# Performance work log

Measured on AMD Instinct MI355X. Metric: run time of the kernel, lower is better.

Reference implementation:

```python
import math
import jax, jax.numpy as jnp
import numpy as np
from jax import lax

C = 64          # channels
N = 16          # d_state
EXPAND = 2
DI = C * EXPAND # d_inner = 128
K = 4           # d_conv
DT_RANK = math.ceil(C / 16)  # 4


def setup_inputs() -> dict:
    key = jax.random.key(0)
    ks = jax.random.split(key, 8)
    B, D, H, W = 1, 48, 48, 48
    s = 0.02
    x = jax.random.normal(ks[0], (B, C, D, H, W), jnp.float32)
    # stacked params for the 3 directional MambaBlocks (z, y, x)
    in_proj = jax.random.normal(ks[1], (3, 2 * DI, C), jnp.float32) * s
    conv_w = jax.random.normal(ks[2], (3, DI, 1, K), jnp.float32) * s
    conv_b = jnp.zeros((3, DI), jnp.float32)
    x_proj = jax.random.normal(ks[3], (3, DT_RANK + 2 * N, DI), jnp.float32) * s
    dt_w = jax.random.normal(ks[4], (3, DI, DT_RANK), jnp.float32) * s
    dt_b = jax.random.normal(ks[5], (3, DI), jnp.float32) * s
    A_log = jnp.log(jnp.broadcast_to(jnp.arange(1, N + 1, dtype=jnp.float32), (3, DI, N)))
    D_ssm = jnp.ones((3, DI), jnp.float32)
    out_proj = jax.random.normal(ks[6], (3, C, DI), jnp.float32) * s
    ln_g = jnp.ones((3, C), jnp.float32)
    ln_b = jnp.zeros((3, C), jnp.float32)
    alpha = jnp.ones((3,), jnp.float32)
    return dict(x=x, in_proj=in_proj, conv_w=conv_w, conv_b=conv_b, x_proj=x_proj,
                dt_w=dt_w, dt_b=dt_b, A_log=A_log, D_ssm=D_ssm, out_proj=out_proj,
                ln_g=ln_g, ln_b=ln_b, alpha=alpha)


def _layer_norm(x, g, b, eps=1e-5):
    m = x.mean(-1, keepdims=True)
    v = ((x - m) ** 2).mean(-1, keepdims=True)
    return (x - m) * lax.rsqrt(v + eps) * g + b


def _mamba(xs, in_w, cw, cb, xp, dtw, dtb, a_log, d_p, ow):
    # xs: (b, l, C)
    b, l, _ = xs.shape
    xr = xs @ in_w.T                              # (b, l, 2*DI)
    xin, res = jnp.split(xr, 2, axis=-1)
    # depthwise causal conv1d (torch pads K-1 both sides then slices [:l])
    xc = lax.conv_general_dilated(xin, cw.transpose(2, 1, 0), (1,), [(K - 1, 0)],
                                  dimension_numbers=('NWC', 'WIO', 'NWC'),
                                  feature_group_count=DI) + cb
    u = jax.nn.silu(xc)                           # (b, l, DI)
    x_dbl = u @ xp.T                              # (b, l, DT_RANK + 2N)
    dlt = x_dbl[..., :DT_RANK]
    Bm = x_dbl[..., DT_RANK:DT_RANK + N]
    Cm = x_dbl[..., DT_RANK + N:]
    delta = jax.nn.softplus(dlt @ dtw.T + dtb)    # (b, l, DI)
    A = -jnp.exp(a_log)                           # (DI, N)

    def step(h, inp):
        d_t, B_t, C_t, u_t = inp                  # (b,DI),(b,N),(b,N),(b,DI)
        h = jnp.exp(d_t[:, :, None] * A) * h + (d_t * u_t)[:, :, None] * B_t[:, None, :]
        return h, jnp.einsum('bdn,bn->bd', h, C_t)

    h0 = jnp.zeros((b, DI, N), xs.dtype)
    _, ys = lax.scan(step, h0, (jnp.swapaxes(delta, 0, 1), jnp.swapaxes(Bm, 0, 1),
                                jnp.swapaxes(Cm, 0, 1), jnp.swapaxes(u, 0, 1)))
    y = jnp.swapaxes(ys, 0, 1) + u * d_p          # (b, l, DI)
    y = y * jax.nn.silu(res)
    return y @ ow.T                               # (b, l, C)


def reference(x, in_proj, conv_w, conv_b, x_proj, dt_w, dt_b, A_log, D_ssm,
              out_proj, ln_g, ln_b, alpha):
    B, Cc, D, H, W = x.shape

    def run(i, xseq):
        xn = _layer_norm(xseq, ln_g[i], ln_b[i])
        return _mamba(xn, in_proj[i], conv_w[i], conv_b[i], x_proj[i],
                      dt_w[i], dt_b[i], A_log[i], D_ssm[i], out_proj[i])

    xz = run(0, x.transpose(0, 3, 4, 2, 1).reshape(B * H * W, D, Cc))
    xz = xz.reshape(B, H, W, D, Cc).transpose(0, 4, 3, 1, 2)
    xy = run(1, x.transpose(0, 2, 4, 3, 1).reshape(B * D * W, H, Cc))
    xy = xy.reshape(B, D, W, H, Cc).transpose(0, 4, 1, 3, 2)
    xx = run(2, x.transpose(0, 2, 3, 4, 1).reshape(B * D * H, W, Cc))
    xx = xx.reshape(B, D, H, W, Cc).transpose(0, 4, 1, 2, 3)
    w = jax.nn.softmax(alpha)
    return w[0] * xz + w[1] * xy + w[2] * xx
```

## Files before the change

kernel.cpp:

```cpp
#include <hip/hip_runtime.h>
#include <math.h>


#define CS   110592
#define L2E  1.44269504088896340736f

#define IPT_OFF  (110592 * 256)
#define OPT_OFF  (IPT_OFF + 3 * 64 * 256)
#define WS_FLOATS (OPT_OFF + 3 * 128 * 64)

__device__ __forceinline__ float fast_silu(float x) {
    return x / (1.0f + __expf(-x));
}

__global__ void prep_kernel(const float* __restrict__ ip,
                            const float* __restrict__ op,
                            float* __restrict__ ws)
{
    float* ipT = ws + IPT_OFF;
    float* opT = ws + OPT_OFF;
    int i = blockIdx.x * 256 + threadIdx.x;
    if (i < 3 * 256 * 64) {
        int dir = i / 16384, r = i % 16384, j = r / 64, c = r % 64;
        ipT[dir * 16384 + c * 256 + j] = ip[i];
    } else {
        int k = i - 3 * 256 * 64;
        if (k < 3 * 64 * 128) {
            int dir = k / 8192, r = k % 8192, c = r / 128, dch = r % 128;
            opT[dir * 8192 + dch * 64 + c] = op[k];
        }
    }
}

template<int DIR>
__global__ __launch_bounds__(256, 4)
void k1_lnproj(const float* __restrict__ x,
               const float* __restrict__ ln_g,
               const float* __restrict__ ln_b,
               float* __restrict__ ws)
{
    __shared__ float Xs[64 * 64];
    const float* ipT = ws + IPT_OFF + DIR * 16384;
    float* tb = ws;
    const int tid = threadIdx.x;
    const int p0 = blockIdx.x * 64;

    {
        const int c0 = tid >> 6, j = tid & 63;
#pragma unroll
        for (int cc = 0; cc < 16; cc++) {
            int c = cc * 4 + c0;
            Xs[c * 64 + j] = x[c * CS + p0 + j];
        }
    }
    __syncthreads();

    if (tid < 64) {
        float s1 = 0.f, s2 = 0.f;
#pragma unroll
        for (int c = 0; c < 64; c++) {
            float v = Xs[c * 64 + tid];
            s1 += v; s2 += v * v;
        }
        float m  = s1 * (1.f / 64.f);
        float rs = rsqrtf(s2 * (1.f / 64.f) - m * m + 1e-5f);
#pragma unroll
        for (int c = 0; c < 64; c++) {
            Xs[c * 64 + tid] = (Xs[c * 64 + tid] - m) * rs * ln_g[DIR * 64 + c]
                               + ln_b[DIR * 64 + c];
        }
    }
    __syncthreads();

    float wgt[64];
#pragma unroll
    for (int c = 0; c < 64; c++) wgt[c] = ipT[c * 256 + tid];

    for (int g = 0; g < 4; g++) {
        float acc[16];
#pragma unroll
        for (int i = 0; i < 16; i++) acc[i] = 0.f;
#pragma unroll 8
        for (int c = 0; c < 64; c++) {
            const float4* xr = (const float4*)&Xs[c * 64 + g * 16];
            float4 x0 = xr[0], x1 = xr[1], x2 = xr[2], x3 = xr[3];
            float wv = wgt[c];
            acc[0]  += x0.x * wv; acc[1]  += x0.y * wv;
            acc[2]  += x0.z * wv; acc[3]  += x0.w * wv;
            acc[4]  += x1.x * wv; acc[5]  += x1.y * wv;
            acc[6]  += x1.z * wv; acc[7]  += x1.w * wv;
            acc[8]  += x2.x * wv; acc[9]  += x2.y * wv;
            acc[10] += x2.z * wv; acc[11] += x2.w * wv;
            acc[12] += x3.x * wv; acc[13] += x3.y * wv;
            acc[14] += x3.z * wv; acc[15] += x3.w * wv;
        }
        if (tid >= 128) {
#pragma unroll
            for (int i = 0; i < 16; i++) acc[i] = fast_silu(acc[i]);
        }
#pragma unroll
        for (int i = 0; i < 16; i++) {
            int p = p0 + g * 16 + i;
            int d_sp = p / 2304, rem = p % 2304;
            int h = rem / 48, w = rem % 48;
            int tau;
            if (DIR == 0)      tau = rem * 48 + d_sp;
            else if (DIR == 1) tau = (d_sp * 48 + w) * 48 + h;
            else               tau = (d_sp * 48 + h) * 48 + w;
            tb[tau * 256 + tid] = acc[i];
        }
    }
}

template<int DIR>
__global__ __launch_bounds__(128, 2)
void k2_scan(const float* __restrict__ conv_w,
             const float* __restrict__ conv_b,
             const float* __restrict__ x_proj,
             const float* __restrict__ dt_w,
             const float* __restrict__ dt_b,
             const float* __restrict__ A_log,
             const float* __restrict__ D_ssm,
             float* __restrict__ ws)
{
    __shared__ float u_s[48 * 132];
    __shared__ float xd_s[48 * 44];
    float* tb = ws;
    const int tid = threadIdx.x;
    const int t0 = blockIdx.x * (48 * 256);

    {
        const int d = tid;
        float xin[48];
#pragma unroll
        for (int t = 0; t < 48; t++) xin[t] = tb[t0 + t * 256 + d];
        float4 cw = *(const float4*)(conv_w + DIR * 512 + d * 4);
        float cb  = conv_b[DIR * 128 + d];
#pragma unroll
        for (int t = 0; t < 48; t++) {
            float a0 = (t >= 3) ? xin[t-3] : 0.f;
            float a1 = (t >= 2) ? xin[t-2] : 0.f;
            float a2 = (t >= 1) ? xin[t-1] : 0.f;
            float v = cw.x * a0 + cw.y * a1 + cw.z * a2 + cw.w * xin[t] + cb;
            u_s[t * 132 + d] = fast_silu(v);
        }
    }
    __syncthreads();

    {
        const int t = tid & 63;
        const int wv = __builtin_amdgcn_readfirstlane(tid >> 6);
        if (t < 48) {
            float acc[18];
#pragma unroll
            for (int j = 0; j < 18; j++) acc[j] = 0.f;
            const float* xpw = x_proj + DIR * 36 * 128 + (wv * 18) * 128;
#pragma unroll
            for (int qc = 0; qc < 4; qc++) {
                float4 u4[8];
                const float4* urow = (const float4*)&u_s[t * 132 + qc * 32];
#pragma unroll
                for (int q = 0; q < 8; q++) u4[q] = urow[q];
#pragma unroll
                for (int j = 0; j < 18; j++) {
                    const float4* wr = (const float4*)(xpw + j * 128 + qc * 32);
                    float a0 = 0.f, a1 = 0.f, a2 = 0.f, a3 = 0.f;
#pragma unroll
                    for (int q = 0; q < 8; q++) {
                        float4 w4 = wr[q];
                        a0 += u4[q].x * w4.x; a1 += u4[q].y * w4.y;
                        a2 += u4[q].z * w4.z; a3 += u4[q].w * w4.w;
                    }
                    acc[j] += (a0 + a1) + (a2 + a3);
                }
            }
#pragma unroll
            for (int j = 0; j < 18; j++) xd_s[t * 44 + wv * 18 + j] = acc[j];
        }
    }
    __syncthreads();

    {
        const int d = tid;
        float A2[16]; bool powok = true;
#pragma unroll
        for (int n = 0; n < 16; n++) {
            float a = -__expf(A_log[DIR * 2048 + d * 16 + n]);
            powok = powok && (fabsf(a + (float)(n + 1)) < 1e-3f);
            A2[n] = a * L2E;
        }
        float4 dtw = *(const float4*)(dt_w + DIR * 512 + d * 4);
        float dtbv = dt_b[DIR * 128 + d];
        float dsv  = D_ssm[DIR * 128 + d];
        float h[16];
#pragma unroll
        for (int n = 0; n < 16; n++) h[n] = 0.f;

#define HN(n, Bc, Cc) h[n] = e[n] * h[n] + du * (Bc); y += h[n] * (Cc);
#define SCAN_BODY(EXP_BLOCK)                                                   \
        for (int tt = 0; tt < 48; tt++) {                                      \
            const float4* xr4 = (const float4*)&xd_s[tt * 44];                 \
            float4 dv = xr4[0];                                                \
            float uu = u_s[tt * 132 + d];                                      \
            float dl = dtbv + dtw.x*dv.x + dtw.y*dv.y + dtw.z*dv.z + dtw.w*dv.w; \
            float delta = (dl > 20.f) ? dl : log1pf(__expf(dl));               \
            float du = delta * uu;                                             \
            float e[16];                                                       \
            EXP_BLOCK                                                          \
            float4 B0 = xr4[1], B1 = xr4[2], B2 = xr4[3], B3 = xr4[4];         \
            float4 C0 = xr4[5], C1 = xr4[6], C2 = xr4[7], C3 = xr4[8];         \
            float y = 0.f;                                                     \
            HN(0,  B0.x, C0.x) HN(1,  B0.y, C0.y)                              \
            HN(2,  B0.z, C0.z) HN(3,  B0.w, C0.w)                              \
            HN(4,  B1.x, C1.x) HN(5,  B1.y, C1.y)                              \
            HN(6,  B1.z, C1.z) HN(7,  B1.w, C1.w)                              \
            HN(8,  B2.x, C2.x) HN(9,  B2.y, C2.y)                              \
            HN(10, B2.z, C2.z) HN(11, B2.w, C2.w)                              \
            HN(12, B3.x, C3.x) HN(13, B3.y, C3.y)                              \
            HN(14, B3.z, C3.z) HN(15, B3.w, C3.w)                              \
            tb[t0 + tt * 256 + d] = y + uu * dsv;                              \
        }

        if (powok) {
            SCAN_BODY({
                float p = exp2f(-delta * L2E);
                e[0] = p;
                _Pragma("unroll")
                for (int n = 1; n < 16; n++) e[n] = e[n-1] * p;
            })
        } else {
            SCAN_BODY({
                _Pragma("unroll")
                for (int n = 0; n < 16; n++) e[n] = exp2f(delta * A2[n]);
            })
        }
#undef SCAN_BODY
#undef HN
    }
}

template<int DIR, bool FIRST>
__global__ __launch_bounds__(128, 4)
void k3_outproj(const float* __restrict__ alpha,
                float* __restrict__ ws,
                float* __restrict__ out)
{
    __shared__ float sb[48 * 132];
    float* tb = ws;
    const float* opT = ws + OPT_OFF + DIR * 8192;
    const int tid = threadIdx.x;
    const int b = blockIdx.x;
    const int d_sp = b / 48;
    const int h = b - d_sp * 48;

    float a0 = alpha[0], a1 = alpha[1], a2 = alpha[2];
    float mx = fmaxf(a0, fmaxf(a1, a2));
    float e0 = __expf(a0 - mx), e1 = __expf(a1 - mx), e2 = __expf(a2 - mx);
    float wdir = ((DIR == 0) ? e0 : (DIR == 1) ? e1 : e2) / (e0 + e1 + e2);

#pragma unroll 4
    for (int w = 0; w < 48; w++) {
        int tau;
        if (DIR == 0)      tau = (h * 48 + w) * 48 + d_sp;
        else if (DIR == 1) tau = (d_sp * 48 + w) * 48 + h;
        else               tau = (d_sp * 48 + h) * 48 + w;
        float zv = tb[tau * 256 + tid];
        float rv = tb[tau * 256 + 128 + tid];
        sb[w * 132 + tid] = zv * rv;
    }
    __syncthreads();

    const int cp = tid & 31;
    const int wg = tid >> 5;
    float acc0[12], acc1[12];
#pragma unroll
    for (int i = 0; i < 12; i++) { acc0[i] = 0.f; acc1[i] = 0.f; }
#pragma unroll 2
    for (int dc = 0; dc < 32; dc++) {
        float w0[4], w1[4];
#pragma unroll
        for (int i = 0; i < 4; i++) {
            w0[i] = opT[(dc * 4 + i) * 64 + cp];
            w1[i] = opT[(dc * 4 + i) * 64 + cp + 32];
        }
#pragma unroll
        for (int i = 0; i < 12; i++) {
            int w = wg * 12 + i;
            float4 z4 = *(const float4*)&sb[w * 132 + dc * 4];
            acc0[i] += z4.x * w0[0] + z4.y * w0[1] + z4.z * w0[2] + z4.w * w0[3];
            acc1[i] += z4.x * w1[0] + z4.y * w1[1] + z4.z * w1[2] + z4.w * w1[3];
        }
    }
    __syncthreads();
#pragma unroll
    for (int i = 0; i < 12; i++) {
        int w = wg * 12 + i;
        sb[cp * 49 + w]        = acc0[i];
        sb[(cp + 32) * 49 + w] = acc1[i];
    }
    __syncthreads();
    const int obase = d_sp * 2304 + h * 48;
    for (int o = tid; o < 3072; o += 128) {
        int c = o / 48, w = o - c * 48;
        int addr = c * CS + obase + w;
        float val = wdir * sb[c * 49 + w];
        if (!FIRST) val += out[addr];
        out[addr] = val;
    }
}

template<int DIR, bool FIRST>
__global__ __launch_bounds__(128, 2)
void mamba_dir_v1(const float* __restrict__ x, const float* __restrict__ in_proj,
                  const float* __restrict__ conv_w, const float* __restrict__ conv_b,
                  const float* __restrict__ x_proj, const float* __restrict__ dt_w,
                  const float* __restrict__ dt_b, const float* __restrict__ A_log,
                  const float* __restrict__ D_ssm, const float* __restrict__ out_proj,
                  const float* __restrict__ ln_g, const float* __restrict__ ln_b,
                  const float* __restrict__ alpha, float* __restrict__ out)
{
    __shared__ float xs_s[48 * 68];
    __shared__ float u_s[48 * 128];
    __shared__ float xd_s[48 * 40];
    const int tid = threadIdx.x;
    const int lane = tid & 63;
    const int wv = __builtin_amdgcn_readfirstlane(tid >> 6);
    const int s = blockIdx.x;
    int base, TS;
    if (DIR == 0)      { base = s;                               TS = 2304; }
    else if (DIR == 1) { base = (s / 48) * 2304 + (s % 48);      TS = 48;   }
    else               { base = (s / 48) * 2304 + (s % 48) * 48; TS = 1;    }
    const float* ip = in_proj + DIR * 256 * 64;
    const float* xp = x_proj + DIR * 36 * 128;
    const float* op = out_proj + DIR * 64 * 128;
    float a0 = alpha[0], a1 = alpha[1], a2 = alpha[2];
    float mx = fmaxf(a0, fmaxf(a1, a2));
    float e0 = __expf(a0 - mx), e1 = __expf(a1 - mx), e2 = __expf(a2 - mx);
    float wdir = ((DIR == 0) ? e0 : (DIR == 1) ? e1 : e2) / (e0 + e1 + e2);
    for (int o = tid; o < 48 * 64; o += 128) {
        int t = o % 48, c = o / 48;
        xs_s[t * 68 + c] = x[c * CS + base + t * TS];
    }
    __syncthreads();
    const int t = lane;
    float xr[64];
    if (t < 48) {
        const float4* row = (const float4*)&xs_s[t * 68];
#pragma unroll
        for (int q = 0; q < 16; q++) {
            float4 v = row[q];
            xr[4*q+0]=v.x; xr[4*q+1]=v.y; xr[4*q+2]=v.z; xr[4*q+3]=v.w;
        }
        float m = 0.f;
#pragma unroll
        for (int c = 0; c < 64; c++) m += xr[c];
        m *= (1.0f / 64.0f);
        float var = 0.f;
#pragma unroll
        for (int c = 0; c < 64; c++) { float d0 = xr[c] - m; var += d0 * d0; }
        var *= (1.0f / 64.0f);
        float rs = rsqrtf(var + 1e-5f);
#pragma unroll
        for (int c = 0; c < 64; c++)
            xr[c] = (xr[c] - m) * rs * ln_g[DIR * 64 + c] + ln_b[DIR * 64 + c];
    }
    __syncthreads();
    if (t < 48 && wv == 0) {
        float4* row = (float4*)&xs_s[t * 68];
#pragma unroll
        for (int q = 0; q < 16; q++) {
            float4 v; v.x=xr[4*q+0]; v.y=xr[4*q+1]; v.z=xr[4*q+2]; v.w=xr[4*q+3];
            row[q] = v;
        }
    }
    if (t < 48) {
        for (int jj = 0; jj < 64; jj++) {
            int j = wv * 64 + jj;
            const float4* wrow = (const float4*)(ip + j * 64);
            float acc = 0.f;
#pragma unroll
            for (int q = 0; q < 16; q++) {
                float4 w4 = wrow[q];
                acc += xr[4*q+0]*w4.x + xr[4*q+1]*w4.y + xr[4*q+2]*w4.z + xr[4*q+3]*w4.w;
            }
            int col = (((j >> 2) ^ (t & 7)) << 2) | (j & 3);
            u_s[t * 128 + col] = acc;
        }
    }
    __syncthreads();
    {
        const int d = tid;
        float4 cw = *(const float4*)(conv_w + DIR * 512 + d * 4);
        float cb = conv_b[DIR * 128 + d];
        float w0 = 0.f, w1 = 0.f, w2 = 0.f;
        for (int tt = 0; tt < 48; tt++) {
            int col = tt * 128 + ((((d >> 2) ^ (tt & 7)) << 2) | (d & 3));
            float w3 = u_s[col];
            float xc = cw.x*w0 + cw.y*w1 + cw.z*w2 + cw.w*w3 + cb;
            u_s[col] = fast_silu(xc);
            w0 = w1; w1 = w2; w2 = w3;
        }
    }
    __syncthreads();
    if (t < 48) {
        float ur[128];
        const float4* urow = (const float4*)&u_s[t * 128];
#pragma unroll
        for (int g = 0; g < 32; g++) {
            float4 v = urow[g ^ (t & 7)];
            ur[4*g]=v.x; ur[4*g+1]=v.y; ur[4*g+2]=v.z; ur[4*g+3]=v.w;
        }
        for (int jj = 0; jj < 18; jj++) {
            int j = wv * 18 + jj;
            const float4* wrow = (const float4*)(xp + j * 128);
            float acc = 0.f;
#pragma unroll
            for (int q = 0; q < 32; q++) {
                float4 w4 = wrow[q];
                acc += ur[4*q]*w4.x + ur[4*q+1]*w4.y + ur[4*q+2]*w4.z + ur[4*q+3]*w4.w;
            }
            xd_s[t * 40 + j] = acc;
        }
    }
    __syncthreads();
    {
        const int d = tid;
        float A2[16]; bool powok = true;
#pragma unroll
        for (int n = 0; n < 16; n++) {
            float a = -__expf(A_log[DIR * 2048 + d * 16 + n]);
            powok = powok && (fabsf(a + (float)(n + 1)) < 1e-3f);
            A2[n] = a * L2E;
        }
        float4 dtw = *(const float4*)(dt_w + DIR * 512 + d * 4);
        float dtbv = dt_b[DIR * 128 + d];
        float dsv = D_ssm[DIR * 128 + d];
        float h[16];
#pragma unroll
        for (int n = 0; n < 16; n++) h[n] = 0.f;
#define SCAN_BODY(EXP_BLOCK)                                                   \
        for (int tt = 0; tt < 48; tt++) {                                      \
            const float* xrow = &xd_s[tt * 40];                                \
            float4 dl4 = *(const float4*)xrow;                                 \
            float dl = dtbv + dtw.x*dl4.x + dtw.y*dl4.y + dtw.z*dl4.z + dtw.w*dl4.w; \
            float delta = (dl > 20.f) ? dl : log1pf(__expf(dl));               \
            int col = tt * 128 + ((((d >> 2) ^ (tt & 7)) << 2) | (d & 3));     \
            float uu = u_s[col];                                               \
            float du = delta * uu;                                             \
            float e[16];                                                       \
            EXP_BLOCK                                                          \
            float4 Bv0 = *(const float4*)(xrow + 4);                           \
            float4 Bv1 = *(const float4*)(xrow + 8);                           \
            float4 Bv2 = *(const float4*)(xrow + 12);                          \
            float4 Bv3 = *(const float4*)(xrow + 16);                          \
            float4 Cv0 = *(const float4*)(xrow + 20);                          \
            float4 Cv1 = *(const float4*)(xrow + 24);                          \
            float4 Cv2 = *(const float4*)(xrow + 28);                          \
            float4 Cv3 = *(const float4*)(xrow + 32);                          \
            float Bf[16] = {Bv0.x,Bv0.y,Bv0.z,Bv0.w, Bv1.x,Bv1.y,Bv1.z,Bv1.w,  \
                            Bv2.x,Bv2.y,Bv2.z,Bv2.w, Bv3.x,Bv3.y,Bv3.z,Bv3.w}; \
            float Cf[16] = {Cv0.x,Cv0.y,Cv0.z,Cv0.w, Cv1.x,Cv1.y,Cv1.z,Cv1.w,  \
                            Cv2.x,Cv2.y,Cv2.z,Cv2.w, Cv3.x,Cv3.y,Cv3.z,Cv3.w}; \
            float y = 0.f;                                                     \
            _Pragma("unroll")                                                  \
            for (int n = 0; n < 16; n++) {                                     \
                h[n] = e[n] * h[n] + du * Bf[n];                               \
                y += h[n] * Cf[n];                                             \
            }                                                                  \
            u_s[col] = y + uu * dsv;                                           \
        }
        if (powok) {
            SCAN_BODY({
                float p = exp2f(-delta * L2E);
                e[0] = p;
                _Pragma("unroll")
                for (int n = 1; n < 16; n++) e[n] = e[n-1] * p;
            })
        } else {
            SCAN_BODY({
                _Pragma("unroll")
                for (int n = 0; n < 16; n++) e[n] = exp2f(delta * A2[n]);
            })
        }
#undef SCAN_BODY
    }
    {
        const int d = tid;
        float wr[64];
        const float4* wrow = (const float4*)(ip + (128 + d) * 64);
#pragma unroll
        for (int q = 0; q < 16; q++) {
            float4 v = wrow[q];
            wr[4*q]=v.x; wr[4*q+1]=v.y; wr[4*q+2]=v.z; wr[4*q+3]=v.w;
        }
        for (int tt = 0; tt < 48; tt++) {
            const float4* xrow = (const float4*)&xs_s[tt * 68];
            float acc = 0.f;
#pragma unroll
            for (int q = 0; q < 16; q++) {
                float4 v = xrow[q];
                acc += v.x*wr[4*q] + v.y*wr[4*q+1] + v.z*wr[4*q+2] + v.w*wr[4*q+3];
            }
            int col = tt * 128 + ((((d >> 2) ^ (tt & 7)) << 2) | (d & 3));
            u_s[col] = u_s[col] * fast_silu(acc);
        }
    }
    __syncthreads();
    if (t < 48) {
        float zr[128];
        const float4* zrow = (const float4*)&u_s[t * 128];
#pragma unroll
        for (int g = 0; g < 32; g++) {
            float4 v = zrow[g ^ (t & 7)];
            zr[4*g]=v.x; zr[4*g+1]=v.y; zr[4*g+2]=v.z; zr[4*g+3]=v.w;
        }
        for (int cc = 0; cc < 32; cc++) {
            int c = wv * 32 + cc;
            const float4* wrow = (const float4*)(op + c * 128);
            float acc = 0.f;
#pragma unroll
            for (int q = 0; q < 32; q++) {
                float4 w4 = wrow[q];
                acc += zr[4*q]*w4.x + zr[4*q+1]*w4.y + zr[4*q+2]*w4.z + zr[4*q+3]*w4.w;
            }
            int oaddr = c * CS + base + t * TS;
            float vout = wdir * acc;
            if (!FIRST) vout += out[oaddr];
            out[oaddr] = vout;
        }
    }
}

extern "C" void kernel_launch(void* const* d_in, const int* in_sizes, int n_in,
                              void* d_out, int out_size, void* d_ws, size_t ws_size,
                              hipStream_t stream) {
    const float* x        = (const float*)d_in[0];
    const float* in_proj  = (const float*)d_in[1];
    const float* conv_w   = (const float*)d_in[2];
    const float* conv_b   = (const float*)d_in[3];
    const float* x_proj   = (const float*)d_in[4];
    const float* dt_w     = (const float*)d_in[5];
    const float* dt_b     = (const float*)d_in[6];
    const float* A_log    = (const float*)d_in[7];
    const float* D_ssm    = (const float*)d_in[8];
    const float* out_proj = (const float*)d_in[9];
    const float* ln_g     = (const float*)d_in[10];
    const float* ln_b     = (const float*)d_in[11];
    const float* alpha    = (const float*)d_in[12];
    float* out = (float*)d_out;
    float* ws  = (float*)d_ws;

    if (ws_size >= (size_t)WS_FLOATS * 4) {
        prep_kernel<<<288, 256, 0, stream>>>(in_proj, out_proj, ws);

        k1_lnproj<0><<<1728, 256, 0, stream>>>(x, ln_g, ln_b, ws);
        k2_scan<0><<<2304, 128, 0, stream>>>(conv_w, conv_b, x_proj, dt_w, dt_b, A_log, D_ssm, ws);
        k3_outproj<0, true ><<<2304, 128, 0, stream>>>(alpha, ws, out);

        k1_lnproj<1><<<1728, 256, 0, stream>>>(x, ln_g, ln_b, ws);
        k2_scan<1><<<2304, 128, 0, stream>>>(conv_w, conv_b, x_proj, dt_w, dt_b, A_log, D_ssm, ws);
        k3_outproj<1, false><<<2304, 128, 0, stream>>>(alpha, ws, out);

        k1_lnproj<2><<<1728, 256, 0, stream>>>(x, ln_g, ln_b, ws);
        k2_scan<2><<<2304, 128, 0, stream>>>(conv_w, conv_b, x_proj, dt_w, dt_b, A_log, D_ssm, ws);
        k3_outproj<2, false><<<2304, 128, 0, stream>>>(alpha, ws, out);
    } else {
        dim3 grid(2304), block(128);
        mamba_dir_v1<0, true ><<<grid, block, 0, stream>>>(x, in_proj, conv_w, conv_b, x_proj,
            dt_w, dt_b, A_log, D_ssm, out_proj, ln_g, ln_b, alpha, out);
        mamba_dir_v1<1, false><<<grid, block, 0, stream>>>(x, in_proj, conv_w, conv_b, x_proj,
            dt_w, dt_b, A_log, D_ssm, out_proj, ln_g, ln_b, alpha, out);
        mamba_dir_v1<2, false><<<grid, block, 0, stream>>>(x, in_proj, conv_w, conv_b, x_proj,
            dt_w, dt_b, A_log, D_ssm, out_proj, ln_g, ln_b, alpha, out);
    }
}
```

Baseline: 1.128 ms.

## Recompute gate projection in outproj and halve the intermediate buffer

k1 now computes only the 128 x-branch channels and stores them in natural spatial order at 128 floats per position, instead of 256 in a scan-transposed order. k3 recomputes layernorm and the gate (res) half of the in_proj so that half no longer round-trips through global memory. k2 reads its 48-step sequences with a direction-dependent stride, uses an XOR-swizzled shared layout instead of padding, and computes exp per state with a branch-free softplus, dropping the power-chain fast path. The intent is to cut global memory traffic, at the cost of extra recomputation, strided loads in k2, and more transcendentals in the scan.

```diff
diff --git a/kernel.cpp b/kernel.cpp
--- a/kernel.cpp
+++ b/kernel.cpp
@@ -3,14 +3,17 @@
 
 
 #define CS   110592
-#define L2E  1.44269504088896340736f
-
-#define IPT_OFF  (110592 * 256)
+#define TBF  (110592 * 128)
+#define IPT_OFF  TBF
 #define OPT_OFF  (IPT_OFF + 3 * 64 * 256)
 #define WS_FLOATS (OPT_OFF + 3 * 128 * 64)
 
 __device__ __forceinline__ float fast_silu(float x) {
     return x / (1.0f + __expf(-x));
+}
+__device__ __forceinline__ float softplus_f(float x) {
+    float em = __expf(-fabsf(x));
+    return fmaxf(x, 0.f) + __logf(1.f + em);
 }
 
 __global__ void prep_kernel(const float* __restrict__ ip,
@@ -72,11 +75,14 @@
     }
     __syncthreads();
 
+    const int ch = tid & 127, half = tid >> 7;
     float wgt[64];
 #pragma unroll
-    for (int c = 0; c < 64; c++) wgt[c] = ipT[c * 256 + tid];
-
-    for (int g = 0; g < 4; g++) {
+    for (int c = 0; c < 64; c++) wgt[c] = ipT[c * 256 + ch];
+
+#pragma unroll
+    for (int gg = 0; gg < 2; gg++) {
+        int g = half * 2 + gg;
         float acc[16];
 #pragma unroll
         for (int i = 0; i < 16; i++) acc[i] = 0.f;
@@ -94,21 +100,9 @@
             acc[12] += x3.x * wv; acc[13] += x3.y * wv;
             acc[14] += x3.z * wv; acc[15] += x3.w * wv;
         }
-        if (tid >= 128) {
-#pragma unroll
-            for (int i = 0; i < 16; i++) acc[i] = fast_silu(acc[i]);
-        }
-#pragma unroll
-        for (int i = 0; i < 16; i++) {
-            int p = p0 + g * 16 + i;
-            int d_sp = p / 2304, rem = p % 2304;
-            int h = rem / 48, w = rem % 48;
-            int tau;
-            if (DIR == 0)      tau = rem * 48 + d_sp;
-            else if (DIR == 1) tau = (d_sp * 48 + w) * 48 + h;
-            else               tau = (d_sp * 48 + h) * 48 + w;
-            tb[tau * 256 + tid] = acc[i];
-        }
+#pragma unroll
+        for (int i = 0; i < 16; i++)
+            tb[(size_t)(p0 + g * 16 + i) * 128 + ch] = acc[i];
     }
 }
 
@@ -123,17 +117,23 @@
              const float* __restrict__ D_ssm,
              float* __restrict__ ws)
 {
-    __shared__ float u_s[48 * 132];
-    __shared__ float xd_s[48 * 44];
+    __shared__ float u_s[48 * 128];
+    __shared__ float xd_s[48 * 36];
     float* tb = ws;
     const int tid = threadIdx.x;
-    const int t0 = blockIdx.x * (48 * 256);
+    const int s = blockIdx.x;
+
+    int base, TS;
+    if (DIR == 0)      { base = s;                               TS = 2304; }
+    else if (DIR == 1) { base = (s / 48) * 2304 + (s % 48);      TS = 48;   }
+    else               { base = (s / 48) * 2304 + (s % 48) * 48; TS = 1;    }
 
     {
         const int d = tid;
         float xin[48];
 #pragma unroll
-        for (int t = 0; t < 48; t++) xin[t] = tb[t0 + t * 256 + d];
+        for (int t = 0; t < 48; t++)
+            xin[t] = tb[(size_t)(base + t * TS) * 128 + d];
         float4 cw = *(const float4*)(conv_w + DIR * 512 + d * 4);
         float cb  = conv_b[DIR * 128 + d];
 #pragma unroll
@@ -142,52 +142,57 @@
             float a1 = (t >= 2) ? xin[t-2] : 0.f;
             float a2 = (t >= 1) ? xin[t-1] : 0.f;
             float v = cw.x * a0 + cw.y * a1 + cw.z * a2 + cw.w * xin[t] + cb;
-            u_s[t * 132 + d] = fast_silu(v);
-        }
-    }
-    __syncthreads();
-
-    {
-        const int t = tid & 63;
+            u_s[t * 128 + (((((d >> 2) ^ (t & 7))) << 2) | (d & 3))] = fast_silu(v);
+        }
+    }
+    __syncthreads();
+
+    {
+        const int t  = tid & 63;
         const int wv = __builtin_amdgcn_readfirstlane(tid >> 6);
+        const int tr = (t < 48) ? t : 47;
+        const int sw = tr & 7;
+        float acc[18];
+#pragma unroll
+        for (int j = 0; j < 18; j++) acc[j] = 0.f;
+        const float* xpw = x_proj + DIR * 36 * 128 + (wv * 18) * 128;
+        const float4* urow = (const float4*)&u_s[tr * 128];
+#pragma unroll
+        for (int qc = 0; qc < 4; qc++) {
+            float4 u4[8];
+#pragma unroll
+            for (int q = 0; q < 8; q++) u4[q] = urow[qc * 8 + (q ^ sw)];
+#pragma unroll
+            for (int j = 0; j < 18; j++) {
+                const float4* wr = (const float4*)(xpw + j * 128 + qc * 32);
+                float a0 = 0.f, a1 = 0.f, a2 = 0.f, a3 = 0.f;
+#pragma unroll
+                for (int q = 0; q < 8; q++) {
+                    float4 w4 = wr[q];
+                    a0 += u4[q].x * w4.x; a1 += u4[q].y * w4.y;
+                    a2 += u4[q].z * w4.z; a3 += u4[q].w * w4.w;
+                }
+                acc[j] += (a0 + a1) + (a2 + a3);
+            }
+        }
         if (t < 48) {
-            float acc[18];
-#pragma unroll
-            for (int j = 0; j < 18; j++) acc[j] = 0.f;
-            const float* xpw = x_proj + DIR * 36 * 128 + (wv * 18) * 128;
-#pragma unroll
-            for (int qc = 0; qc < 4; qc++) {
-                float4 u4[8];
-                const float4* urow = (const float4*)&u_s[t * 132 + qc * 32];
-#pragma unroll
-                for (int q = 0; q < 8; q++) u4[q] = urow[q];
-#pragma unroll
-                for (int j = 0; j < 18; j++) {
-                    const float4* wr = (const float4*)(xpw + j * 128 + qc * 32);
-                    float a0 = 0.f, a1 = 0.f, a2 = 0.f, a3 = 0.f;
-#pragma unroll
-                    for (int q = 0; q < 8; q++) {
-                        float4 w4 = wr[q];
-                        a0 += u4[q].x * w4.x; a1 += u4[q].y * w4.y;
-                        a2 += u4[q].z * w4.z; a3 += u4[q].w * w4.w;
-                    }
-                    acc[j] += (a0 + a1) + (a2 + a3);
-                }
-            }
-#pragma unroll
-            for (int j = 0; j < 18; j++) xd_s[t * 44 + wv * 18 + j] = acc[j];
+#pragma unroll
+            for (int j = 0; j < 18; j++) xd_s[t * 36 + wv * 18 + j] = acc[j];
         }
     }
     __syncthreads();
 
     {
         const int d = tid;
-        float A2[16]; bool powok = true;
-#pragma unroll
-        for (int n = 0; n < 16; n++) {
-            float a = -__expf(A_log[DIR * 2048 + d * 16 + n]);
-            powok = powok && (fabsf(a + (float)(n + 1)) < 1e-3f);
-            A2[n] = a * L2E;
+        float A[16];
+        {
+            const float4* al = (const float4*)(A_log + DIR * 2048 + d * 16);
+#pragma unroll
+            for (int q = 0; q < 4; q++) {
+                float4 v = al[q];
+                A[4*q+0] = -__expf(v.x); A[4*q+1] = -__expf(v.y);
+                A[4*q+2] = -__expf(v.z); A[4*q+3] = -__expf(v.w);
+            }
         }
         float4 dtw = *(const float4*)(dt_w + DIR * 512 + d * 4);
         float dtbv = dt_b[DIR * 128 + d];
@@ -196,77 +201,112 @@
 #pragma unroll
         for (int n = 0; n < 16; n++) h[n] = 0.f;
 
-#define HN(n, Bc, Cc) h[n] = e[n] * h[n] + du * (Bc); y += h[n] * (Cc);
-#define SCAN_BODY(EXP_BLOCK)                                                   \
-        for (int tt = 0; tt < 48; tt++) {                                      \
-            const float4* xr4 = (const float4*)&xd_s[tt * 44];                 \
-            float4 dv = xr4[0];                                                \
-            float uu = u_s[tt * 132 + d];                                      \
-            float dl = dtbv + dtw.x*dv.x + dtw.y*dv.y + dtw.z*dv.z + dtw.w*dv.w; \
-            float delta = (dl > 20.f) ? dl : log1pf(__expf(dl));               \
-            float du = delta * uu;                                             \
-            float e[16];                                                       \
-            EXP_BLOCK                                                          \
-            float4 B0 = xr4[1], B1 = xr4[2], B2 = xr4[3], B3 = xr4[4];         \
-            float4 C0 = xr4[5], C1 = xr4[6], C2 = xr4[7], C3 = xr4[8];         \
-            float y = 0.f;                                                     \
-            HN(0,  B0.x, C0.x) HN(1,  B0.y, C0.y)                              \
-            HN(2,  B0.z, C0.z) HN(3,  B0.w, C0.w)                              \
-            HN(4,  B1.x, C1.x) HN(5,  B1.y, C1.y)                              \
-            HN(6,  B1.z, C1.z) HN(7,  B1.w, C1.w)                              \
-            HN(8,  B2.x, C2.x) HN(9,  B2.y, C2.y)                              \
-            HN(10, B2.z, C2.z) HN(11, B2.w, C2.w)                              \
-            HN(12, B3.x, C3.x) HN(13, B3.y, C3.y)                              \
-            HN(14, B3.z, C3.z) HN(15, B3.w, C3.w)                              \
-            tb[t0 + tt * 256 + d] = y + uu * dsv;                              \
-        }
-
-        if (powok) {
-            SCAN_BODY({
-                float p = exp2f(-delta * L2E);
-                e[0] = p;
-                _Pragma("unroll")
-                for (int n = 1; n < 16; n++) e[n] = e[n-1] * p;
-            })
-        } else {
-            SCAN_BODY({
-                _Pragma("unroll")
-                for (int n = 0; n < 16; n++) e[n] = exp2f(delta * A2[n]);
-            })
-        }
-#undef SCAN_BODY
+        const int dsw_hi = d >> 2, dlo = d & 3;
+        for (int tt = 0; tt < 48; tt++) {
+            const float4* xr4 = (const float4*)&xd_s[tt * 36];
+            float4 R0 = xr4[0];
+            float uu = u_s[tt * 128 + (((dsw_hi ^ (tt & 7)) << 2) | dlo)];
+            float dl = dtbv + dtw.x*R0.x + dtw.y*R0.y + dtw.z*R0.z + dtw.w*R0.w;
+            float delta = softplus_f(dl);
+            float du = delta * uu;
+            float4 B0 = xr4[1], B1 = xr4[2], B2 = xr4[3], B3 = xr4[4];
+            float4 C0 = xr4[5], C1 = xr4[6], C2 = xr4[7], C3 = xr4[8];
+            float y0 = 0.f, y1 = 0.f, y2 = 0.f, y3 = 0.f;
+#define HN(n, Bc, Cc, ya) { float e = __expf(delta * A[n]); \
+            h[n] = e * h[n] + du * (Bc); ya += h[n] * (Cc); }
+            HN(0,  B0.x, C0.x, y0) HN(1,  B0.y, C0.y, y1)
+            HN(2,  B0.z, C0.z, y2) HN(3,  B0.w, C0.w, y3)
+            HN(4,  B1.x, C1.x, y0) HN(5,  B1.y, C1.y, y1)
+            HN(6,  B1.z, C1.z, y2) HN(7,  B1.w, C1.w, y3)
+            HN(8,  B2.x, C2.x, y0) HN(9,  B2.y, C2.y, y1)
+            HN(10, B2.z, C2.z, y2) HN(11, B2.w, C2.w, y3)
+            HN(12, B3.x, C3.x, y0) HN(13, B3.y, C3.y, y1)
+            HN(14, B3.z, C3.z, y2) HN(15, B3.w, C3.w, y3)
 #undef HN
+            tb[(size_t)(base + tt * TS) * 128 + d] =
+                ((y0 + y1) + (y2 + y3)) + uu * dsv;
+        }
     }
 }
 
 template<int DIR, bool FIRST>
 __global__ __launch_bounds__(128, 4)
-void k3_outproj(const float* __restrict__ alpha,
+void k3_outproj(const float* __restrict__ x,
+                const float* __restrict__ ln_g,
+                const float* __restrict__ ln_b,
+                const float* __restrict__ alpha,
                 float* __restrict__ ws,
                 float* __restrict__ out)
 {
     __shared__ float sb[48 * 132];
+    __shared__ float xs[64 * 52];
     float* tb = ws;
+    const float* ipT = ws + IPT_OFF + DIR * 16384;
     const float* opT = ws + OPT_OFF + DIR * 8192;
     const int tid = threadIdx.x;
     const int b = blockIdx.x;
     const int d_sp = b / 48;
     const int h = b - d_sp * 48;
+    const int obase = d_sp * 2304 + h * 48;
 
     float a0 = alpha[0], a1 = alpha[1], a2 = alpha[2];
     float mx = fmaxf(a0, fmaxf(a1, a2));
     float e0 = __expf(a0 - mx), e1 = __expf(a1 - mx), e2 = __expf(a2 - mx);
     float wdir = ((DIR == 0) ? e0 : (DIR == 1) ? e1 : e2) / (e0 + e1 + e2);
 
-#pragma unroll 4
-    for (int w = 0; w < 48; w++) {
-        int tau;
-        if (DIR == 0)      tau = (h * 48 + w) * 48 + d_sp;
-        else if (DIR == 1) tau = (d_sp * 48 + w) * 48 + h;
-        else               tau = (d_sp * 48 + h) * 48 + w;
-        float zv = tb[tau * 256 + tid];
-        float rv = tb[tau * 256 + 128 + tid];
-        sb[w * 132 + tid] = zv * rv;
+    for (int o = tid; o < 64 * 48; o += 128) {
+        int c = o / 48, w = o - c * 48;
+        xs[c * 52 + w] = x[c * CS + obase + w];
+    }
+    __syncthreads();
+
+    if (tid < 48) {
+        const int w = tid;
+        float s1 = 0.f, s2 = 0.f;
+#pragma unroll
+        for (int c = 0; c < 64; c++) {
+            float v = xs[c * 52 + w];
+            s1 += v; s2 += v * v;
+        }
+        float m  = s1 * (1.f / 64.f);
+        float rs = rsqrtf(s2 * (1.f / 64.f) - m * m + 1e-5f);
+#pragma unroll
+        for (int c = 0; c < 64; c++) {
+            xs[c * 52 + w] = (xs[c * 52 + w] - m) * rs * ln_g[DIR * 64 + c]
+                             + ln_b[DIR * 64 + c];
+        }
+    }
+    __syncthreads();
+
+    {
+        const int d = tid;
+        float wgt2[64];
+#pragma unroll
+        for (int c = 0; c < 64; c++) wgt2[c] = ipT[c * 256 + 128 + d];
+#pragma unroll
+        for (int wb = 0; wb < 4; wb++) {
+            float acc[12];
+#pragma unroll
+            for (int i = 0; i < 12; i++) acc[i] = 0.f;
+#pragma unroll 8
+            for (int c = 0; c < 64; c++) {
+                const float4* xr = (const float4*)&xs[c * 52 + wb * 12];
+                float4 v0 = xr[0], v1 = xr[1], v2 = xr[2];
+                float wv = wgt2[c];
+                acc[0] += v0.x * wv; acc[1] += v0.y * wv;
+                acc[2] += v0.z * wv; acc[3] += v0.w * wv;
+                acc[4] += v1.x * wv; acc[5] += v1.y * wv;
+                acc[6] += v1.z * wv; acc[7] += v1.w * wv;
+                acc[8] += v2.x * wv; acc[9] += v2.y * wv;
+                acc[10] += v2.z * wv; acc[11] += v2.w * wv;
+            }
+#pragma unroll
+            for (int i = 0; i < 12; i++) {
+                int w = wb * 12 + i;
+                float zv = tb[(size_t)(obase + w) * 128 + d];
+                sb[w * 132 + d] = zv * fast_silu(acc[i]);
+            }
+        }
     }
     __syncthreads();
 
@@ -299,7 +339,6 @@
         sb[(cp + 32) * 49 + w] = acc1[i];
     }
     __syncthreads();
-    const int obase = d_sp * 2304 + h * 48;
     for (int o = tid; o < 3072; o += 128) {
         int c = o / 48, w = o - c * 48;
         int addr = c * CS + obase + w;
@@ -430,7 +469,7 @@
         for (int n = 0; n < 16; n++) {
             float a = -__expf(A_log[DIR * 2048 + d * 16 + n]);
             powok = powok && (fabsf(a + (float)(n + 1)) < 1e-3f);
-            A2[n] = a * L2E;
+            A2[n] = a * 1.44269504088896340736f;
         }
         float4 dtw = *(const float4*)(dt_w + DIR * 512 + d * 4);
         float dtbv = dt_b[DIR * 128 + d];
@@ -471,7 +510,7 @@
         }
         if (powok) {
             SCAN_BODY({
-                float p = exp2f(-delta * L2E);
+                float p = exp2f(-delta * 1.44269504088896340736f);
                 e[0] = p;
                 _Pragma("unroll")
                 for (int n = 1; n < 16; n++) e[n] = e[n-1] * p;
@@ -555,15 +594,15 @@
 
         k1_lnproj<0><<<1728, 256, 0, stream>>>(x, ln_g, ln_b, ws);
         k2_scan<0><<<2304, 128, 0, stream>>>(conv_w, conv_b, x_proj, dt_w, dt_b, A_log, D_ssm, ws);
-        k3_outproj<0, true ><<<2304, 128, 0, stream>>>(alpha, ws, out);
+        k3_outproj<0, true ><<<2304, 128, 0, stream>>>(x, ln_g, ln_b, alpha, ws, out);
 
         k1_lnproj<1><<<1728, 256, 0, stream>>>(x, ln_g, ln_b, ws);
         k2_scan<1><<<2304, 128, 0, stream>>>(conv_w, conv_b, x_proj, dt_w, dt_b, A_log, D_ssm, ws);
-        k3_outproj<1, false><<<2304, 128, 0, stream>>>(alpha, ws, out);
+        k3_outproj<1, false><<<2304, 128, 0, stream>>>(x, ln_g, ln_b, alpha, ws, out);
 
         k1_lnproj<2><<<1728, 256, 0, stream>>>(x, ln_g, ln_b, ws);
         k2_scan<2><<<2304, 128, 0, stream>>>(conv_w, conv_b, x_proj, dt_w, dt_b, A_log, D_ssm, ws);
-        k3_outproj<2, false><<<2304, 128, 0, stream>>>(alpha, ws, out);
+        k3_outproj<2, false><<<2304, 128, 0, stream>>>(x, ln_g, ln_b, alpha, ws, out);
     } else {
         dim3 grid(2304), block(128);
         mamba_dir_v1<0, true ><<<grid, block, 0, stream>>>(x, in_proj, conv_w, conv_b, x_proj,
```

Result: no change. 1.136 ms (+0.7%).
